# Optimization experiments

Measured on AMD Instinct MI355X. Metric: run time of the kernel, lower is better.

## Reference

```python
import jax, jax.numpy as jnp
import numpy as np

B, S, D, H = 2, 2048, 1024, 16
DEPTH = D // H
NEG = -1.0e9


def setup_inputs() -> dict:
    key = jax.random.key(0)
    ks = jax.random.split(key, 12)
    s = 1.0 / np.sqrt(D)
    return {
        "q": jax.random.normal(ks[0], (B, S, D), jnp.float32),
        "k": jax.random.normal(ks[1], (B, S, D), jnp.float32),
        "v": jax.random.normal(ks[2], (B, S, D), jnp.float32),
        "mask": jax.random.randint(ks[3], (B, 1, 1, S), 0, 2).astype(jnp.float32),
        "wq": jax.random.normal(ks[4], (D, D), jnp.float32) * s,
        "bq": jnp.zeros((D,), jnp.float32),
        "wk": jax.random.normal(ks[5], (D, D), jnp.float32) * s,
        "bk": jnp.zeros((D,), jnp.float32),
        "wv": jax.random.normal(ks[6], (D, D), jnp.float32) * s,
        "bv": jnp.zeros((D,), jnp.float32),
        "wo": jax.random.normal(ks[7], (D, D), jnp.float32) * s,
        "bo": jnp.zeros((D,), jnp.float32),
    }


def _split_heads(x):
    # [B, S, D] -> [B, H, S, depth]
    b, s, _ = x.shape
    return x.reshape(b, s, H, DEPTH).transpose(0, 2, 1, 3)


def reference(q, k, v, mask, wq, bq, wk, bk, wv, bv, wo, bo):
    qh = _split_heads(q @ wq + bq)
    kh = _split_heads(k @ wk + bk)
    vh = _split_heads(v @ wv + bv)
    scale = 1.0 / jnp.sqrt(jnp.asarray(DEPTH, jnp.float32))
    logits = jnp.einsum("bhqd,bhkd->bhqk", qh, kh) * scale
    logits = logits + mask * NEG
    attn = jax.nn.softmax(logits, axis=-1)  # [B, H, Sq, Skv]
    out = jnp.einsum("bhqk,bhkd->bhqd", attn, vh)
    out = out.transpose(0, 2, 1, 3).reshape(q.shape[0], -1, D)
    out = out @ wo + bo
    return out, attn
```

## Files before the change

### kernel.cpp

```cpp
#include <hip/hip_runtime.h>

typedef unsigned short u16;
typedef unsigned int   u32;
typedef __bf16 bf16x8 __attribute__((ext_vector_type(8)));
typedef float  f32x4  __attribute__((ext_vector_type(4)));
typedef u16    u16x8  __attribute__((ext_vector_type(8)));

#define S_   2048
#define D_   1024
#define H_   16
#define M_   4096

#define SCALE2 0.18033688011112042f
#define MASKC  (-1.4426950408889634e9f)
#define SHIFT2 11.541560327111707f

__device__ __forceinline__ u16 f2b(float f){
  union { float f; u32 i; } x; x.f = f;
  u32 u = x.i;
  u32 r = (u + 0x7fffu + ((u >> 16) & 1u)) >> 16;
  return (u16)r;
}
__device__ __forceinline__ void async16(u16* lds, const u16* g){
  __builtin_amdgcn_global_load_lds((const __attribute__((address_space(1))) void*)g,
                                   (__attribute__((address_space(3))) void*)lds, 16, 0, 0);
}
__device__ __forceinline__ f32x4 mma16(bf16x8 a, bf16x8 b, f32x4 c){
  return __builtin_amdgcn_mfma_f32_16x16x32_bf16(a, b, c, 0, 0, 0);
}
__device__ __forceinline__ bf16x8 ld_frag_u16(const u16* p){
  u16x8 v = *(const u16x8*)p;
  return __builtin_bit_cast(bf16x8, v);
}

__global__ __launch_bounds__(256) void prep(
    const float* __restrict__ q, const float* __restrict__ k, const float* __restrict__ v,
    u16* __restrict__ qb, u16* __restrict__ kb, u16* __restrict__ vb,
    const float* __restrict__ w0, const float* __restrict__ w1,
    const float* __restrict__ w2, const float* __restrict__ w3,
    u16* __restrict__ t0, u16* __restrict__ t1,
    u16* __restrict__ t2, u16* __restrict__ t3)
{
  const int bid = blockIdx.x;
  if (bid < 6144){
    const int which = bid >> 11;
    const int bx = bid & 2047;
    const float* x = (which == 0) ? q : (which == 1) ? k : v;
    u16* y = (which == 0) ? qb : (which == 1) ? kb : vb;
    size_t i = (size_t)bx * 256 + threadIdx.x;
    const f32x4* p = (const f32x4*)(x + i * 8);
    f32x4 a = p[0], b = p[1];
    u16x8 o;
    o[0] = f2b(a[0]); o[1] = f2b(a[1]); o[2] = f2b(a[2]); o[3] = f2b(a[3]);
    o[4] = f2b(b[0]); o[5] = f2b(b[1]); o[6] = f2b(b[2]); o[7] = f2b(b[3]);
    *(u16x8*)(y + i * 8) = o;
  } else {
    const int b = bid - 6144;
    const int z = b >> 8, rem = b & 255, by = rem >> 4, bx = rem & 15;
    const float* W; u16* T;
    switch (z){
      case 0: W = w0; T = t0; break;
      case 1: W = w1; T = t1; break;
      case 2: W = w2; T = t2; break;
      default: W = w3; T = t3; break;
    }
    __shared__ u16 tile[64][65];
    const int t = threadIdx.x;
    const int r0 = by * 64, c0 = bx * 64;
    const int row = t >> 2, cg = t & 3;
    const float* src = W + (size_t)(r0 + row) * D_ + c0 + cg * 16;
    f32x4 a0 = *(const f32x4*)(src + 0);
    f32x4 a1 = *(const f32x4*)(src + 4);
    f32x4 a2 = *(const f32x4*)(src + 8);
    f32x4 a3 = *(const f32x4*)(src + 12);
    #pragma unroll
    for (int e = 0; e < 4; ++e){
      tile[row][cg*16 +      e] = f2b(a0[e]);
      tile[row][cg*16 +  4 + e] = f2b(a1[e]);
      tile[row][cg*16 +  8 + e] = f2b(a2[e]);
      tile[row][cg*16 + 12 + e] = f2b(a3[e]);
    }
    __syncthreads();
    u16* dst = T + (size_t)(c0 + row) * D_ + r0 + cg * 16;
    u16x8 oa, ob;
    #pragma unroll
    for (int e = 0; e < 8; ++e){ oa[e] = tile[cg*16 + e][row]; ob[e] = tile[cg*16 + 8 + e][row]; }
    *(u16x8*)dst = oa;
    *(u16x8*)(dst + 8) = ob;
  }
}

__global__ __launch_bounds__(256) void gemm_qkv(
    const u16* __restrict__ qb, const u16* __restrict__ kb, const u16* __restrict__ vb,
    const u16* __restrict__ wqT, const u16* __restrict__ wkT, const u16* __restrict__ wvT,
    const float* __restrict__ bq, const float* __restrict__ bk, const float* __restrict__ bv,
    u16* __restrict__ Qh, u16* __restrict__ Kh, u16* __restrict__ Vt)
{
  __shared__ __attribute__((aligned(16))) u16 As[128 * 64];
  __shared__ __attribute__((aligned(16))) u16 Bs[128 * 64];
  const u16 *A, *Bt; const float* bias; u16* Cb;
  switch (blockIdx.z){
    case 0: A = qb; Bt = wqT; bias = bq; Cb = Qh; break;
    case 1: A = kb; Bt = wkT; bias = bk; Cb = Kh; break;
    default: A = vb; Bt = wvT; bias = bv; Cb = Vt; break;
  }
  const bool vtr = (blockIdx.z == 2);
  const int tid = threadIdx.x;
  const int wave = tid >> 6, lane = tid & 63, ln = lane & 15, quad = lane >> 4;
  const int wm = wave >> 1, wn = wave & 1;
  const int m0 = blockIdx.x * 128, n0 = blockIdx.y * 128;

  f32x4 acc[4][4];
  #pragma unroll
  for (int i = 0; i < 4; ++i)
    #pragma unroll
    for (int j = 0; j < 4; ++j) acc[i][j] = (f32x4){0.f, 0.f, 0.f, 0.f};

  for (int kt = 0; kt < D_; kt += 64){
    #pragma unroll
    for (int it = 0; it < 4; ++it){
      int i = it * 256 + tid;
      int r = i >> 3, c = i & 7, cs = c ^ (r & 7);
      async16(&As[i * 8], &A [(size_t)(m0 + r) * D_ + kt + cs * 8]);
      async16(&Bs[i * 8], &Bt[(size_t)(n0 + r) * D_ + kt + cs * 8]);
    }
    __syncthreads();
    #pragma unroll
    for (int kk = 0; kk < 2; ++kk){
      bf16x8 af[4], bfr[4];
      #pragma unroll
      for (int i4 = 0; i4 < 4; ++i4){
        int row = wm * 64 + i4 * 16 + ln;
        af[i4] = ld_frag_u16(&As[row * 64 + ((kk * 4 + quad) ^ (row & 7)) * 8]);
      }
      #pragma unroll
      for (int j4 = 0; j4 < 4; ++j4){
        int row = wn * 64 + j4 * 16 + ln;
        bfr[j4] = ld_frag_u16(&Bs[row * 64 + ((kk * 4 + quad) ^ (row & 7)) * 8]);
      }
      #pragma unroll
      for (int i4 = 0; i4 < 4; ++i4)
        #pragma unroll
        for (int j4 = 0; j4 < 4; ++j4)
          acc[i4][j4] = mma16(af[i4], bfr[j4], acc[i4][j4]);
    }
    __syncthreads();
  }

  #pragma unroll
  for (int j4 = 0; j4 < 4; ++j4){
    int nidx = n0 + wn * 64 + j4 * 16 + ln;
    float biasv = bias[nidx];
    #pragma unroll
    for (int i4 = 0; i4 < 4; ++i4){
      #pragma unroll
      for (int rg = 0; rg < 4; ++rg){
        int r = m0 + wm * 64 + i4 * 16 + quad * 4 + rg;
        float val = acc[i4][j4][rg] + biasv;
        int bb = r >> 11, s = r & 2047, hh = nidx >> 6, dc = nidx & 63;
        size_t idx = vtr ? (((size_t)(bb * H_ + hh) * 64 + dc) * S_ + s)
                         : (((size_t)(bb * H_ + hh) * S_ + s) * 64 + dc);
        Cb[idx] = f2b(val);
      }
    }
  }
}

__global__ __launch_bounds__(256) void gemm_o(
    const u16* __restrict__ A, const u16* __restrict__ Bt,
    const float* __restrict__ bias, float* __restrict__ Cf)
{
  __shared__ __attribute__((aligned(16))) u16 As[2][128 * 64];
  __shared__ __attribute__((aligned(16))) u16 Bs[2][128 * 64];
  const int tid = threadIdx.x;
  const int wave = tid >> 6, lane = tid & 63, ln = lane & 15, quad = lane >> 4;
  const int wm = wave >> 1, wn = wave & 1;
  const int m0 = blockIdx.x * 128, n0 = blockIdx.y * 128;

  f32x4 acc[4][4];
  #pragma unroll
  for (int i = 0; i < 4; ++i)
    #pragma unroll
    for (int j = 0; j < 4; ++j) acc[i][j] = (f32x4){0.f, 0.f, 0.f, 0.f};

  #pragma unroll
  for (int it = 0; it < 4; ++it){
    int i = it * 256 + tid;
    int r = i >> 3, c = i & 7, cs = c ^ (r & 7);
    async16(&As[0][i * 8], &A [(size_t)(m0 + r) * D_ + cs * 8]);
    async16(&Bs[0][i * 8], &Bt[(size_t)(n0 + r) * D_ + cs * 8]);
  }
  __syncthreads();

  int cur = 0;
  for (int kt = 0; kt < D_; kt += 64){
    if (kt + 64 < D_){
      int nb = cur ^ 1;
      #pragma unroll
      for (int it = 0; it < 4; ++it){
        int i = it * 256 + tid;
        int r = i >> 3, c = i & 7, cs = c ^ (r & 7);
        async16(&As[nb][i * 8], &A [(size_t)(m0 + r) * D_ + kt + 64 + cs * 8]);
        async16(&Bs[nb][i * 8], &Bt[(size_t)(n0 + r) * D_ + kt + 64 + cs * 8]);
      }
    }
    #pragma unroll
    for (int kk = 0; kk < 2; ++kk){
      bf16x8 af[4], bfr[4];
      #pragma unroll
      for (int i4 = 0; i4 < 4; ++i4){
        int row = wm * 64 + i4 * 16 + ln;
        af[i4] = ld_frag_u16(&As[cur][row * 64 + ((kk * 4 + quad) ^ (row & 7)) * 8]);
      }
      #pragma unroll
      for (int j4 = 0; j4 < 4; ++j4){
        int row = wn * 64 + j4 * 16 + ln;
        bfr[j4] = ld_frag_u16(&Bs[cur][row * 64 + ((kk * 4 + quad) ^ (row & 7)) * 8]);
      }
      #pragma unroll
      for (int i4 = 0; i4 < 4; ++i4)
        #pragma unroll
        for (int j4 = 0; j4 < 4; ++j4)
          acc[i4][j4] = mma16(af[i4], bfr[j4], acc[i4][j4]);
    }
    __syncthreads();
    cur ^= 1;
  }

  #pragma unroll
  for (int j4 = 0; j4 < 4; ++j4){
    int nidx = n0 + wn * 64 + j4 * 16 + ln;
    float biasv = bias[nidx];
    #pragma unroll
    for (int i4 = 0; i4 < 4; ++i4){
      #pragma unroll
      for (int rg = 0; rg < 4; ++rg){
        int r = m0 + wm * 64 + i4 * 16 + quad * 4 + rg;
        Cf[(size_t)r * D_ + nidx] = acc[i4][j4][rg] + biasv;
      }
    }
  }
}

__global__ __launch_bounds__(256) void attn_stats(
    const u16* __restrict__ Qh, const u16* __restrict__ Kh,
    const float* __restrict__ maskp, float* __restrict__ lrow)
{
  __shared__ __attribute__((aligned(16))) u16 Qs[64 * 64];
  __shared__ __attribute__((aligned(16))) u16 Ks[2][64 * 64];
  const int tid = threadIdx.x;
  const int wave = tid >> 6, lane = tid & 63, ln = lane & 15, quad = lane >> 4;
  const int q0 = blockIdx.x * 64;
  const int bh = blockIdx.y;
  const int bsel = bh >> 4;

  #pragma unroll
  for (int it = 0; it < 2; ++it){
    int i = it * 256 + tid;
    int r = i >> 3, c = i & 7, cs = c ^ (r & 7);
    async16(&Qs[i * 8],    &Qh[((size_t)bh * S_ + q0 + r) * 64 + cs * 8]);
    async16(&Ks[0][i * 8], &Kh[((size_t)bh * S_ + r) * 64 + cs * 8]);
  }
  __syncthreads();
  bf16x8 aq0, aq1;
  {
    int row = wave * 16 + ln;
    aq0 = ld_frag_u16(&Qs[row * 64 + ((0 + quad) ^ (row & 7)) * 8]);
    aq1 = ld_frag_u16(&Qs[row * 64 + ((4 + quad) ^ (row & 7)) * 8]);
  }

  float lsum[4] = {0.f, 0.f, 0.f, 0.f};
  int cur = 0;
  for (int n0 = 0; n0 < S_; n0 += 64){
    if (n0 + 64 < S_){
      int nb = cur ^ 1;
      #pragma unroll
      for (int it = 0; it < 2; ++it){
        int i = it * 256 + tid;
        int r = i >> 3, c = i & 7, cs = c ^ (r & 7);
        async16(&Ks[nb][i * 8], &Kh[((size_t)bh * S_ + n0 + 64 + r) * 64 + cs * 8]);
      }
    }
    float mv[4];
    #pragma unroll
    for (int j = 0; j < 4; ++j)
      mv[j] = maskp[bsel * S_ + n0 + j * 16 + ln] * MASKC - SHIFT2;
    #pragma unroll
    for (int j = 0; j < 4; ++j){
      int row = j * 16 + ln;
      bf16x8 b0 = ld_frag_u16(&Ks[cur][row * 64 + ((0 + quad) ^ (row & 7)) * 8]);
      bf16x8 b1 = ld_frag_u16(&Ks[cur][row * 64 + ((4 + quad) ^ (row & 7)) * 8]);
      f32x4 a = {0.f, 0.f, 0.f, 0.f};
      a = mma16(aq0, b0, a);
      a = mma16(aq1, b1, a);
      #pragma unroll
      for (int rg = 0; rg < 4; ++rg)
        lsum[rg] += exp2f(a[rg] * SCALE2 + mv[j]);
    }
    __syncthreads();
    cur ^= 1;
  }
  #pragma unroll
  for (int rg = 0; rg < 4; ++rg){
    float s = lsum[rg];
    s += __shfl_xor(s, 1);
    s += __shfl_xor(s, 2);
    s += __shfl_xor(s, 4);
    s += __shfl_xor(s, 8);
    if (ln == 0)
      lrow[bh * S_ + q0 + wave * 16 + quad * 4 + rg] = s;
  }
}

__global__ __launch_bounds__(256) void attn_pv(
    const u16* __restrict__ Qh, const u16* __restrict__ Kh, const u16* __restrict__ Vt,
    const float* __restrict__ maskp, const float* __restrict__ lrow,
    float* __restrict__ attn, u16* __restrict__ OH)
{
  __shared__ __attribute__((aligned(16))) u16 Qs[64 * 64];
  __shared__ __attribute__((aligned(16))) u16 Ks[2][64 * 64];
  __shared__ __attribute__((aligned(16))) u16 Vs[2][64 * 64];
  __shared__ __attribute__((aligned(16))) u16 Ps[4][16 * 72];
  const int tid = threadIdx.x;
  const int wave = tid >> 6, lane = tid & 63, ln = lane & 15, quad = lane >> 4;
  const int q0 = blockIdx.x * 64;
  const int bh = blockIdx.y;
  const int bsel = bh >> 4;

  #pragma unroll
  for (int it = 0; it < 2; ++it){
    int i = it * 256 + tid;
    int r = i >> 3, c = i & 7, cs = c ^ (r & 7);
    async16(&Qs[i * 8],    &Qh[((size_t)bh * S_ + q0 + r) * 64 + cs * 8]);
    async16(&Ks[0][i * 8], &Kh[((size_t)bh * S_ + r) * 64 + cs * 8]);
    async16(&Vs[0][i * 8], &Vt[((size_t)bh * 64 + r) * S_ + cs * 8]);
  }
  __syncthreads();
  bf16x8 aq0, aq1;
  {
    int row = wave * 16 + ln;
    aq0 = ld_frag_u16(&Qs[row * 64 + ((0 + quad) ^ (row & 7)) * 8]);
    aq1 = ld_frag_u16(&Qs[row * 64 + ((4 + quad) ^ (row & 7)) * 8]);
  }
  float il4[4];
  #pragma unroll
  for (int rg = 0; rg < 4; ++rg){
    int row = q0 + wave * 16 + quad * 4 + rg;
    il4[rg] = 1.0f / lrow[bh * S_ + row];
  }
  f32x4 oacc[4];
  #pragma unroll
  for (int jd = 0; jd < 4; ++jd) oacc[jd] = (f32x4){0.f, 0.f, 0.f, 0.f};

  int cur = 0;
  for (int n0 = 0; n0 < S_; n0 += 64){
    if (n0 + 64 < S_){
      int nb = cur ^ 1;
      #pragma unroll
      for (int it = 0; it < 2; ++it){
        int i = it * 256 + tid;
        int r = i >> 3, c = i & 7, cs = c ^ (r & 7);
        async16(&Ks[nb][i * 8], &Kh[((size_t)bh * S_ + n0 + 64 + r) * 64 + cs * 8]);
        async16(&Vs[nb][i * 8], &Vt[((size_t)bh * 64 + r) * S_ + n0 + 64 + cs * 8]);
      }
    }
    float mv[4];
    #pragma unroll
    for (int j = 0; j < 4; ++j)
      mv[j] = maskp[bsel * S_ + n0 + j * 16 + ln] * MASKC - SHIFT2;
    #pragma unroll
    for (int j = 0; j < 4; ++j){
      int row = j * 16 + ln;
      bf16x8 b0 = ld_frag_u16(&Ks[cur][row * 64 + ((0 + quad) ^ (row & 7)) * 8]);
      bf16x8 b1 = ld_frag_u16(&Ks[cur][row * 64 + ((4 + quad) ^ (row & 7)) * 8]);
      f32x4 a = {0.f, 0.f, 0.f, 0.f};
      a = mma16(aq0, b0, a);
      a = mma16(aq1, b1, a);
      #pragma unroll
      for (int rg = 0; rg < 4; ++rg){
        float p = exp2f(a[rg] * SCALE2 + mv[j]) * il4[rg];
        attn[((size_t)bh * S_ + q0 + wave * 16 + quad * 4 + rg) * S_ + n0 + j * 16 + ln] = p;
        Ps[wave][(quad * 4 + rg) * 72 + j * 16 + ln] = f2b(p);
      }
    }
    #pragma unroll
    for (int kk = 0; kk < 2; ++kk){
      bf16x8 pa = ld_frag_u16(&Ps[wave][ln * 72 + kk * 32 + quad * 8]);
      #pragma unroll
      for (int jd = 0; jd < 4; ++jd){
        int row = jd * 16 + ln;
        bf16x8 vb = ld_frag_u16(&Vs[cur][row * 64 + ((kk * 4 + quad) ^ (row & 7)) * 8]);
        oacc[jd] = mma16(pa, vb, oacc[jd]);
      }
    }
    __syncthreads();
    cur ^= 1;
  }
  const int b = bh >> 4, h = bh & 15;
  #pragma unroll
  for (int jd = 0; jd < 4; ++jd){
    #pragma unroll
    for (int rg = 0; rg < 4; ++rg){
      int row = q0 + wave * 16 + quad * 4 + rg;
      OH[((size_t)b * S_ + row) * D_ + h * 64 + jd * 16 + ln] = f2b(oacc[jd][rg]);
    }
  }
}

extern "C" void kernel_launch(void* const* d_in, const int* in_sizes, int n_in,
                              void* d_out, int out_size, void* d_ws, size_t ws_size,
                              hipStream_t stream)
{
  const float* q    = (const float*)d_in[0];
  const float* k    = (const float*)d_in[1];
  const float* v    = (const float*)d_in[2];
  const float* mask = (const float*)d_in[3];
  const float* wq   = (const float*)d_in[4];
  const float* bq   = (const float*)d_in[5];
  const float* wk   = (const float*)d_in[6];
  const float* bk   = (const float*)d_in[7];
  const float* wv   = (const float*)d_in[8];
  const float* bv   = (const float*)d_in[9];
  const float* wo   = (const float*)d_in[10];
  const float* bo   = (const float*)d_in[11];

  char* ws = (char*)d_ws;
  u16* wqT = (u16*)(ws + 0ull);
  u16* wkT = (u16*)(ws + 2097152ull);
  u16* wvT = (u16*)(ws + 4194304ull);
  u16* woT = (u16*)(ws + 6291456ull);
  u16* qb  = (u16*)(ws + 8388608ull);
  u16* kb  = (u16*)(ws + 16777216ull);
  u16* vb  = (u16*)(ws + 25165824ull);
  u16* Qh  = (u16*)(ws + 33554432ull);
  u16* Kh  = (u16*)(ws + 41943040ull);
  u16* Vt  = (u16*)(ws + 50331648ull);
  u16* OH  = (u16*)(ws + 58720256ull);
  float* lrow = (float*)(ws + 67108864ull);

  float* out  = (float*)d_out;
  float* attn = out + 4194304ull;

  prep<<<dim3(7168), 256, 0, stream>>>(q, k, v, qb, kb, vb,
                                       wq, wk, wv, wo, wqT, wkT, wvT, woT);
  gemm_qkv<<<dim3(32, 8, 3), 256, 0, stream>>>(qb, kb, vb, wqT, wkT, wvT,
                                               bq, bk, bv, Qh, Kh, Vt);
  attn_stats<<<dim3(32, 32), 256, 0, stream>>>(Qh, Kh, mask, lrow);
  attn_pv<<<dim3(32, 32), 256, 0, stream>>>(Qh, Kh, Vt, mask, lrow, attn, OH);
  gemm_o<<<dim3(32, 8), 256, 0, stream>>>(OH, woT, bo, out);
}
```

Before: 846.3 us.

## Load attention fragments directly from global memory and add separate V transpose kernel

Measured after the change: 990.1 us. 17.0% more time.

```diff
diff --git a/kernel.cpp b/kernel.cpp
--- a/kernel.cpp
+++ b/kernel.cpp
@@ -94,7 +94,7 @@
     const u16* __restrict__ qb, const u16* __restrict__ kb, const u16* __restrict__ vb,
     const u16* __restrict__ wqT, const u16* __restrict__ wkT, const u16* __restrict__ wvT,
     const float* __restrict__ bq, const float* __restrict__ bk, const float* __restrict__ bv,
-    u16* __restrict__ Qh, u16* __restrict__ Kh, u16* __restrict__ Vt)
+    u16* __restrict__ Qh, u16* __restrict__ Kh, u16* __restrict__ Vh)
 {
   __shared__ __attribute__((aligned(16))) u16 As[128 * 64];
   __shared__ __attribute__((aligned(16))) u16 Bs[128 * 64];
@@ -102,9 +102,8 @@
   switch (blockIdx.z){
     case 0: A = qb; Bt = wqT; bias = bq; Cb = Qh; break;
     case 1: A = kb; Bt = wkT; bias = bk; Cb = Kh; break;
-    default: A = vb; Bt = wvT; bias = bv; Cb = Vt; break;
-  }
-  const bool vtr = (blockIdx.z == 2);
+    default: A = vb; Bt = wvT; bias = bv; Cb = Vh; break;
+  }
   const int tid = threadIdx.x;
   const int wave = tid >> 6, lane = tid & 63, ln = lane & 15, quad = lane >> 4;
   const int wm = wave >> 1, wn = wave & 1;
@@ -158,12 +157,31 @@
         int r = m0 + wm * 64 + i4 * 16 + quad * 4 + rg;
         float val = acc[i4][j4][rg] + biasv;
         int bb = r >> 11, s = r & 2047, hh = nidx >> 6, dc = nidx & 63;
-        size_t idx = vtr ? (((size_t)(bb * H_ + hh) * 64 + dc) * S_ + s)
-                         : (((size_t)(bb * H_ + hh) * S_ + s) * 64 + dc);
-        Cb[idx] = f2b(val);
-      }
-    }
-  }
+        Cb[((size_t)(bb * H_ + hh) * S_ + s) * 64 + dc] = f2b(val);
+      }
+    }
+  }
+}
+
+__global__ __launch_bounds__(256) void vtrans(
+    const u16* __restrict__ Vh, u16* __restrict__ Vt)
+{
+  __shared__ u16 tile[64][72];
+  const int bh = blockIdx.y, s0 = blockIdx.x * 64;
+  const int t = threadIdx.x;
+  const int row = t >> 2, cg = t & 3;
+  const u16* src = Vh + ((size_t)bh * S_ + s0 + row) * 64 + cg * 16;
+  u16x8 a0 = *(const u16x8*)src;
+  u16x8 a1 = *(const u16x8*)(src + 8);
+  #pragma unroll
+  for (int e = 0; e < 8; ++e){ tile[row][cg*16 + e] = a0[e]; tile[row][cg*16 + 8 + e] = a1[e]; }
+  __syncthreads();
+  u16* dst = Vt + ((size_t)bh * 64 + row) * S_ + s0 + cg * 16;
+  u16x8 oa, ob;
+  #pragma unroll
+  for (int e = 0; e < 8; ++e){ oa[e] = tile[cg*16 + e][row]; ob[e] = tile[cg*16 + 8 + e][row]; }
+  *(u16x8*)dst = oa;
+  *(u16x8*)(dst + 8) = ob;
 }
 
 __global__ __launch_bounds__(256) void gemm_o(
@@ -246,59 +264,44 @@
     const u16* __restrict__ Qh, const u16* __restrict__ Kh,
     const float* __restrict__ maskp, float* __restrict__ lrow)
 {
-  __shared__ __attribute__((aligned(16))) u16 Qs[64 * 64];
-  __shared__ __attribute__((aligned(16))) u16 Ks[2][64 * 64];
   const int tid = threadIdx.x;
   const int wave = tid >> 6, lane = tid & 63, ln = lane & 15, quad = lane >> 4;
   const int q0 = blockIdx.x * 64;
   const int bh = blockIdx.y;
   const int bsel = bh >> 4;
 
-  #pragma unroll
-  for (int it = 0; it < 2; ++it){
-    int i = it * 256 + tid;
-    int r = i >> 3, c = i & 7, cs = c ^ (r & 7);
-    async16(&Qs[i * 8],    &Qh[((size_t)bh * S_ + q0 + r) * 64 + cs * 8]);
-    async16(&Ks[0][i * 8], &Kh[((size_t)bh * S_ + r) * 64 + cs * 8]);
-  }
-  __syncthreads();
-  bf16x8 aq0, aq1;
-  {
-    int row = wave * 16 + ln;
-    aq0 = ld_frag_u16(&Qs[row * 64 + ((0 + quad) ^ (row & 7)) * 8]);
-    aq1 = ld_frag_u16(&Qs[row * 64 + ((4 + quad) ^ (row & 7)) * 8]);
-  }
+  const u16* qp = &Qh[((size_t)bh * S_ + q0 + wave * 16 + ln) * 64 + quad * 8];
+  bf16x8 aq0 = ld_frag_u16(qp);
+  bf16x8 aq1 = ld_frag_u16(qp + 32);
+
+  const u16* kp0 = &Kh[((size_t)bh * S_ + ln) * 64 + quad * 8];
+  const u16* kp1 = kp0 + 16 * 64;
+  const u16* kp2 = kp0 + 32 * 64;
+  const u16* kp3 = kp0 + 48 * 64;
+  const float* mp = &maskp[bsel * S_ + ln];
 
   float lsum[4] = {0.f, 0.f, 0.f, 0.f};
-  int cur = 0;
   for (int n0 = 0; n0 < S_; n0 += 64){
-    if (n0 + 64 < S_){
-      int nb = cur ^ 1;
-      #pragma unroll
-      for (int it = 0; it < 2; ++it){
-        int i = it * 256 + tid;
-        int r = i >> 3, c = i & 7, cs = c ^ (r & 7);
-        async16(&Ks[nb][i * 8], &Kh[((size_t)bh * S_ + n0 + 64 + r) * 64 + cs * 8]);
-      }
-    }
-    float mv[4];
-    #pragma unroll
-    for (int j = 0; j < 4; ++j)
-      mv[j] = maskp[bsel * S_ + n0 + j * 16 + ln] * MASKC - SHIFT2;
-    #pragma unroll
-    for (int j = 0; j < 4; ++j){
-      int row = j * 16 + ln;
-      bf16x8 b0 = ld_frag_u16(&Ks[cur][row * 64 + ((0 + quad) ^ (row & 7)) * 8]);
-      bf16x8 b1 = ld_frag_u16(&Ks[cur][row * 64 + ((4 + quad) ^ (row & 7)) * 8]);
-      f32x4 a = {0.f, 0.f, 0.f, 0.f};
-      a = mma16(aq0, b0, a);
-      a = mma16(aq1, b1, a);
-      #pragma unroll
-      for (int rg = 0; rg < 4; ++rg)
-        lsum[rg] += exp2f(a[rg] * SCALE2 + mv[j]);
-    }
-    __syncthreads();
-    cur ^= 1;
+    float mv0 = mp[ 0] * MASKC - SHIFT2;
+    float mv1 = mp[16] * MASKC - SHIFT2;
+    float mv2 = mp[32] * MASKC - SHIFT2;
+    float mv3 = mp[48] * MASKC - SHIFT2;
+    bf16x8 b00 = ld_frag_u16(kp0), b01 = ld_frag_u16(kp0 + 32);
+    bf16x8 b10 = ld_frag_u16(kp1), b11 = ld_frag_u16(kp1 + 32);
+    bf16x8 b20 = ld_frag_u16(kp2), b21 = ld_frag_u16(kp2 + 32);
+    bf16x8 b30 = ld_frag_u16(kp3), b31 = ld_frag_u16(kp3 + 32);
+    f32x4 a0 = {0.f,0.f,0.f,0.f}, a1 = a0, a2 = a0, a3 = a0;
+    a0 = mma16(aq0, b00, a0); a0 = mma16(aq1, b01, a0);
+    a1 = mma16(aq0, b10, a1); a1 = mma16(aq1, b11, a1);
+    a2 = mma16(aq0, b20, a2); a2 = mma16(aq1, b21, a2);
+    a3 = mma16(aq0, b30, a3); a3 = mma16(aq1, b31, a3);
+    #pragma unroll
+    for (int rg = 0; rg < 4; ++rg){
+      lsum[rg] += exp2f(a0[rg] * SCALE2 + mv0) + exp2f(a1[rg] * SCALE2 + mv1)
+                + exp2f(a2[rg] * SCALE2 + mv2) + exp2f(a3[rg] * SCALE2 + mv3);
+    }
+    kp0 += 64 * 64; kp1 += 64 * 64; kp2 += 64 * 64; kp3 += 64 * 64;
+    mp += 64;
   }
   #pragma unroll
   for (int rg = 0; rg < 4; ++rg){
@@ -317,9 +320,6 @@
     const float* __restrict__ maskp, const float* __restrict__ lrow,
     float* __restrict__ attn, u16* __restrict__ OH)
 {
-  __shared__ __attribute__((aligned(16))) u16 Qs[64 * 64];
-  __shared__ __attribute__((aligned(16))) u16 Ks[2][64 * 64];
-  __shared__ __attribute__((aligned(16))) u16 Vs[2][64 * 64];
   __shared__ __attribute__((aligned(16))) u16 Ps[4][16 * 72];
   const int tid = threadIdx.x;
   const int wave = tid >> 6, lane = tid & 63, ln = lane & 15, quad = lane >> 4;
@@ -327,21 +327,10 @@
   const int bh = blockIdx.y;
   const int bsel = bh >> 4;
 
-  #pragma unroll
-  for (int it = 0; it < 2; ++it){
-    int i = it * 256 + tid;
-    int r = i >> 3, c = i & 7, cs = c ^ (r & 7);
-    async16(&Qs[i * 8],    &Qh[((size_t)bh * S_ + q0 + r) * 64 + cs * 8]);
-    async16(&Ks[0][i * 8], &Kh[((size_t)bh * S_ + r) * 64 + cs * 8]);
-    async16(&Vs[0][i * 8], &Vt[((size_t)bh * 64 + r) * S_ + cs * 8]);
-  }
-  __syncthreads();
-  bf16x8 aq0, aq1;
-  {
-    int row = wave * 16 + ln;
-    aq0 = ld_frag_u16(&Qs[row * 64 + ((0 + quad) ^ (row & 7)) * 8]);
-    aq1 = ld_frag_u16(&Qs[row * 64 + ((4 + quad) ^ (row & 7)) * 8]);
-  }
+  const u16* qp = &Qh[((size_t)bh * S_ + q0 + wave * 16 + ln) * 64 + quad * 8];
+  bf16x8 aq0 = ld_frag_u16(qp);
+  bf16x8 aq1 = ld_frag_u16(qp + 32);
+
   float il4[4];
   #pragma unroll
   for (int rg = 0; rg < 4; ++rg){
@@ -352,49 +341,58 @@
   #pragma unroll
   for (int jd = 0; jd < 4; ++jd) oacc[jd] = (f32x4){0.f, 0.f, 0.f, 0.f};
 
-  int cur = 0;
+  const u16* kp0 = &Kh[((size_t)bh * S_ + ln) * 64 + quad * 8];
+  const u16* kp1 = kp0 + 16 * 64;
+  const u16* kp2 = kp0 + 32 * 64;
+  const u16* kp3 = kp0 + 48 * 64;
+  const u16* vp0 = &Vt[((size_t)bh * 64 + ln) * S_ + quad * 8];
+  const u16* vp1 = vp0 + (size_t)16 * S_;
+  const u16* vp2 = vp0 + (size_t)32 * S_;
+  const u16* vp3 = vp0 + (size_t)48 * S_;
+  const float* mp = &maskp[bsel * S_ + ln];
+  float* ap = &attn[((size_t)bh * S_ + q0 + wave * 16 + quad * 4) * S_ + ln];
+  u16* psw = &Ps[wave][(quad * 4) * 72 + ln];
+  const u16* psr = &Ps[wave][ln * 72 + quad * 8];
+
   for (int n0 = 0; n0 < S_; n0 += 64){
-    if (n0 + 64 < S_){
-      int nb = cur ^ 1;
-      #pragma unroll
-      for (int it = 0; it < 2; ++it){
-        int i = it * 256 + tid;
-        int r = i >> 3, c = i & 7, cs = c ^ (r & 7);
-        async16(&Ks[nb][i * 8], &Kh[((size_t)bh * S_ + n0 + 64 + r) * 64 + cs * 8]);
-        async16(&Vs[nb][i * 8], &Vt[((size_t)bh * 64 + r) * S_ + n0 + 64 + cs * 8]);
-      }
-    }
-    float mv[4];
-    #pragma unroll
-    for (int j = 0; j < 4; ++j)
-      mv[j] = maskp[bsel * S_ + n0 + j * 16 + ln] * MASKC - SHIFT2;
-    #pragma unroll
-    for (int j = 0; j < 4; ++j){
-      int row = j * 16 + ln;
-      bf16x8 b0 = ld_frag_u16(&Ks[cur][row * 64 + ((0 + quad) ^ (row & 7)) * 8]);
-      bf16x8 b1 = ld_frag_u16(&Ks[cur][row * 64 + ((4 + quad) ^ (row & 7)) * 8]);
-      f32x4 a = {0.f, 0.f, 0.f, 0.f};
-      a = mma16(aq0, b0, a);
-      a = mma16(aq1, b1, a);
-      #pragma unroll
-      for (int rg = 0; rg < 4; ++rg){
-        float p = exp2f(a[rg] * SCALE2 + mv[j]) * il4[rg];
-        attn[((size_t)bh * S_ + q0 + wave * 16 + quad * 4 + rg) * S_ + n0 + j * 16 + ln] = p;
-        Ps[wave][(quad * 4 + rg) * 72 + j * 16 + ln] = f2b(p);
-      }
+    float mv0 = mp[ 0] * MASKC - SHIFT2;
+    float mv1 = mp[16] * MASKC - SHIFT2;
+    float mv2 = mp[32] * MASKC - SHIFT2;
+    float mv3 = mp[48] * MASKC - SHIFT2;
+    bf16x8 b00 = ld_frag_u16(kp0), b01 = ld_frag_u16(kp0 + 32);
+    bf16x8 b10 = ld_frag_u16(kp1), b11 = ld_frag_u16(kp1 + 32);
+    bf16x8 b20 = ld_frag_u16(kp2), b21 = ld_frag_u16(kp2 + 32);
+    bf16x8 b30 = ld_frag_u16(kp3), b31 = ld_frag_u16(kp3 + 32);
+    f32x4 a0 = {0.f,0.f,0.f,0.f}, a1 = a0, a2 = a0, a3 = a0;
+    a0 = mma16(aq0, b00, a0); a0 = mma16(aq1, b01, a0);
+    a1 = mma16(aq0, b10, a1); a1 = mma16(aq1, b11, a1);
+    a2 = mma16(aq0, b20, a2); a2 = mma16(aq1, b21, a2);
+    a3 = mma16(aq0, b30, a3); a3 = mma16(aq1, b31, a3);
+    #pragma unroll
+    for (int rg = 0; rg < 4; ++rg){
+      float p0 = exp2f(a0[rg] * SCALE2 + mv0) * il4[rg];
+      float p1 = exp2f(a1[rg] * SCALE2 + mv1) * il4[rg];
+      float p2 = exp2f(a2[rg] * SCALE2 + mv2) * il4[rg];
+      float p3 = exp2f(a3[rg] * SCALE2 + mv3) * il4[rg];
+      float* arow = ap + (size_t)rg * S_ + n0;
+      arow[ 0] = p0; arow[16] = p1; arow[32] = p2; arow[48] = p3;
+      u16* pr = psw + rg * 72;
+      pr[ 0] = f2b(p0); pr[16] = f2b(p1); pr[32] = f2b(p2); pr[48] = f2b(p3);
     }
     #pragma unroll
     for (int kk = 0; kk < 2; ++kk){
-      bf16x8 pa = ld_frag_u16(&Ps[wave][ln * 72 + kk * 32 + quad * 8]);
-      #pragma unroll
-      for (int jd = 0; jd < 4; ++jd){
-        int row = jd * 16 + ln;
-        bf16x8 vb = ld_frag_u16(&Vs[cur][row * 64 + ((kk * 4 + quad) ^ (row & 7)) * 8]);
-        oacc[jd] = mma16(pa, vb, oacc[jd]);
-      }
-    }
-    __syncthreads();
-    cur ^= 1;
+      bf16x8 pa = ld_frag_u16(psr + kk * 32);
+      bf16x8 v0 = ld_frag_u16(vp0 + n0 + kk * 32);
+      bf16x8 v1 = ld_frag_u16(vp1 + n0 + kk * 32);
+      bf16x8 v2 = ld_frag_u16(vp2 + n0 + kk * 32);
+      bf16x8 v3 = ld_frag_u16(vp3 + n0 + kk * 32);
+      oacc[0] = mma16(pa, v0, oacc[0]);
+      oacc[1] = mma16(pa, v1, oacc[1]);
+      oacc[2] = mma16(pa, v2, oacc[2]);
+      oacc[3] = mma16(pa, v3, oacc[3]);
+    }
+    kp0 += 64 * 64; kp1 += 64 * 64; kp2 += 64 * 64; kp3 += 64 * 64;
+    mp += 64;
   }
   const int b = bh >> 4, h = bh & 15;
   #pragma unroll
@@ -434,9 +432,10 @@
   u16* vb  = (u16*)(ws + 25165824ull);
   u16* Qh  = (u16*)(ws + 33554432ull);
   u16* Kh  = (u16*)(ws + 41943040ull);
-  u16* Vt  = (u16*)(ws + 50331648ull);
+  u16* Vh  = (u16*)(ws + 50331648ull);
   u16* OH  = (u16*)(ws + 58720256ull);
   float* lrow = (float*)(ws + 67108864ull);
+  u16* Vt  = vb;
 
   float* out  = (float*)d_out;
   float* attn = out + 4194304ull;
@@ -444,7 +443,8 @@
   prep<<<dim3(7168), 256, 0, stream>>>(q, k, v, qb, kb, vb,
                                        wq, wk, wv, wo, wqT, wkT, wvT, woT);
   gemm_qkv<<<dim3(32, 8, 3), 256, 0, stream>>>(qb, kb, vb, wqT, wkT, wvT,
-                                               bq, bk, bv, Qh, Kh, Vt);
+                                               bq, bk, bv, Qh, Kh, Vh);
+  vtrans<<<dim3(32, 32), 256, 0, stream>>>(Vh, Vt);
   attn_stats<<<dim3(32, 32), 256, 0, stream>>>(Qh, Kh, mask, lrow);
   attn_pv<<<dim3(32, 32), 256, 0, stream>>>(Qh, Kh, Vt, mask, lrow, attn, OH);
   gemm_o<<<dim3(32, 8), 256, 0, stream>>>(OH, woT, bo, out);
```

## Double attention query tile, remap blocks per XCD, and stage QKV epilogue via LDS

Applied to the files above, without the earlier changes.

After: 810.5 us. 1.04x faster.

```diff
diff --git a/kernel.cpp b/kernel.cpp
--- a/kernel.cpp
+++ b/kernel.cpp
@@ -96,8 +96,9 @@
     const float* __restrict__ bq, const float* __restrict__ bk, const float* __restrict__ bv,
     u16* __restrict__ Qh, u16* __restrict__ Kh, u16* __restrict__ Vt)
 {
-  __shared__ __attribute__((aligned(16))) u16 As[128 * 64];
-  __shared__ __attribute__((aligned(16))) u16 Bs[128 * 64];
+  __shared__ __attribute__((aligned(16))) u16 smem[128 * 132];
+  u16* As = smem;
+  u16* Bs = smem + 128 * 64;
   const u16 *A, *Bt; const float* bias; u16* Cb;
   switch (blockIdx.z){
     case 0: A = qb; Bt = wqT; bias = bq; Cb = Qh; break;
@@ -149,19 +150,32 @@
 
   #pragma unroll
   for (int j4 = 0; j4 < 4; ++j4){
-    int nidx = n0 + wn * 64 + j4 * 16 + ln;
-    float biasv = bias[nidx];
+    int nl = wn * 64 + j4 * 16 + ln;
+    float biasv = bias[n0 + nl];
     #pragma unroll
     for (int i4 = 0; i4 < 4; ++i4){
       #pragma unroll
       for (int rg = 0; rg < 4; ++rg){
-        int r = m0 + wm * 64 + i4 * 16 + quad * 4 + rg;
-        float val = acc[i4][j4][rg] + biasv;
-        int bb = r >> 11, s = r & 2047, hh = nidx >> 6, dc = nidx & 63;
-        size_t idx = vtr ? (((size_t)(bb * H_ + hh) * 64 + dc) * S_ + s)
-                         : (((size_t)(bb * H_ + hh) * S_ + s) * 64 + dc);
-        Cb[idx] = f2b(val);
-      }
+        int ml = wm * 64 + i4 * 16 + quad * 4 + rg;
+        u16 hv = f2b(acc[i4][j4][rg] + biasv);
+        smem[vtr ? (nl * 132 + ml) : (ml * 132 + nl)] = hv;
+      }
+    }
+  }
+  __syncthreads();
+  const int bb = m0 >> 11, sbase = m0 & 2047;
+  #pragma unroll
+  for (int c = 0; c < 8; ++c){
+    int task = c * 256 + tid;
+    int rr = task >> 4, ch = task & 15;
+    u16x8 val = *(const u16x8*)&smem[rr * 132 + ch * 8];
+    if (vtr){
+      int hh = (n0 + rr) >> 6, dc = (n0 + rr) & 63;
+      *(u16x8*)&Cb[((size_t)(bb * H_ + hh) * 64 + dc) * S_ + sbase + ch * 8] = val;
+    } else {
+      int s = sbase + rr;
+      int nn = n0 + ch * 8, hh = nn >> 6, dc = nn & 63;
+      *(u16x8*)&Cb[((size_t)(bb * H_ + hh) * S_ + s) * 64 + dc] = val;
     }
   }
 }
@@ -246,30 +260,38 @@
     const u16* __restrict__ Qh, const u16* __restrict__ Kh,
     const float* __restrict__ maskp, float* __restrict__ lrow)
 {
-  __shared__ __attribute__((aligned(16))) u16 Qs[64 * 64];
+  __shared__ __attribute__((aligned(16))) u16 Qs[128 * 64];
   __shared__ __attribute__((aligned(16))) u16 Ks[2][64 * 64];
   const int tid = threadIdx.x;
   const int wave = tid >> 6, lane = tid & 63, ln = lane & 15, quad = lane >> 4;
-  const int q0 = blockIdx.x * 64;
-  const int bh = blockIdx.y;
+  const int orig = blockIdx.x;
+  const int xcd = orig & 7, slot = orig >> 3;
+  const int bh = xcd * 4 + (slot >> 4);
+  const int q0 = (slot & 15) * 128;
   const int bsel = bh >> 4;
 
+  #pragma unroll
+  for (int it = 0; it < 4; ++it){
+    int i = it * 256 + tid;
+    int r = i >> 3, c = i & 7, cs = c ^ (r & 7);
+    async16(&Qs[i * 8], &Qh[((size_t)bh * S_ + q0 + r) * 64 + cs * 8]);
+  }
   #pragma unroll
   for (int it = 0; it < 2; ++it){
     int i = it * 256 + tid;
     int r = i >> 3, c = i & 7, cs = c ^ (r & 7);
-    async16(&Qs[i * 8],    &Qh[((size_t)bh * S_ + q0 + r) * 64 + cs * 8]);
     async16(&Ks[0][i * 8], &Kh[((size_t)bh * S_ + r) * 64 + cs * 8]);
   }
   __syncthreads();
-  bf16x8 aq0, aq1;
-  {
-    int row = wave * 16 + ln;
-    aq0 = ld_frag_u16(&Qs[row * 64 + ((0 + quad) ^ (row & 7)) * 8]);
-    aq1 = ld_frag_u16(&Qs[row * 64 + ((4 + quad) ^ (row & 7)) * 8]);
-  }
-
-  float lsum[4] = {0.f, 0.f, 0.f, 0.f};
+  bf16x8 aq[2][2];
+  #pragma unroll
+  for (int f = 0; f < 2; ++f){
+    int row = wave * 32 + f * 16 + ln;
+    aq[f][0] = ld_frag_u16(&Qs[row * 64 + ((0 + quad) ^ (row & 7)) * 8]);
+    aq[f][1] = ld_frag_u16(&Qs[row * 64 + ((4 + quad) ^ (row & 7)) * 8]);
+  }
+
+  float lsum[2][4] = {{0.f,0.f,0.f,0.f},{0.f,0.f,0.f,0.f}};
   int cur = 0;
   for (int n0 = 0; n0 < S_; n0 += 64){
     if (n0 + 64 < S_){
@@ -290,26 +312,31 @@
       int row = j * 16 + ln;
       bf16x8 b0 = ld_frag_u16(&Ks[cur][row * 64 + ((0 + quad) ^ (row & 7)) * 8]);
       bf16x8 b1 = ld_frag_u16(&Ks[cur][row * 64 + ((4 + quad) ^ (row & 7)) * 8]);
-      f32x4 a = {0.f, 0.f, 0.f, 0.f};
-      a = mma16(aq0, b0, a);
-      a = mma16(aq1, b1, a);
-      #pragma unroll
-      for (int rg = 0; rg < 4; ++rg)
-        lsum[rg] += exp2f(a[rg] * SCALE2 + mv[j]);
+      #pragma unroll
+      for (int f = 0; f < 2; ++f){
+        f32x4 a = {0.f, 0.f, 0.f, 0.f};
+        a = mma16(aq[f][0], b0, a);
+        a = mma16(aq[f][1], b1, a);
+        #pragma unroll
+        for (int rg = 0; rg < 4; ++rg)
+          lsum[f][rg] += exp2f(a[rg] * SCALE2 + mv[j]);
+      }
     }
     __syncthreads();
     cur ^= 1;
   }
   #pragma unroll
-  for (int rg = 0; rg < 4; ++rg){
-    float s = lsum[rg];
-    s += __shfl_xor(s, 1);
-    s += __shfl_xor(s, 2);
-    s += __shfl_xor(s, 4);
-    s += __shfl_xor(s, 8);
-    if (ln == 0)
-      lrow[bh * S_ + q0 + wave * 16 + quad * 4 + rg] = s;
-  }
+  for (int f = 0; f < 2; ++f)
+    #pragma unroll
+    for (int rg = 0; rg < 4; ++rg){
+      float s = lsum[f][rg];
+      s += __shfl_xor(s, 1);
+      s += __shfl_xor(s, 2);
+      s += __shfl_xor(s, 4);
+      s += __shfl_xor(s, 8);
+      if (ln == 0)
+        lrow[bh * S_ + q0 + wave * 32 + f * 16 + quad * 4 + rg] = s;
+    }
 }
 
 __global__ __launch_bounds__(256) void attn_pv(
@@ -317,40 +344,46 @@
     const float* __restrict__ maskp, const float* __restrict__ lrow,
     float* __restrict__ attn, u16* __restrict__ OH)
 {
-  __shared__ __attribute__((aligned(16))) u16 Qs[64 * 64];
   __shared__ __attribute__((aligned(16))) u16 Ks[2][64 * 64];
   __shared__ __attribute__((aligned(16))) u16 Vs[2][64 * 64];
-  __shared__ __attribute__((aligned(16))) u16 Ps[4][16 * 72];
+  __shared__ __attribute__((aligned(16))) u16 Ps[4][32 * 72];
   const int tid = threadIdx.x;
   const int wave = tid >> 6, lane = tid & 63, ln = lane & 15, quad = lane >> 4;
-  const int q0 = blockIdx.x * 64;
-  const int bh = blockIdx.y;
+  const int orig = blockIdx.x;
+  const int xcd = orig & 7, slot = orig >> 3;
+  const int bh = xcd * 4 + (slot >> 4);
+  const int q0 = (slot & 15) * 128;
   const int bsel = bh >> 4;
+
+  bf16x8 aq[2][2];
+  #pragma unroll
+  for (int f = 0; f < 2; ++f){
+    const u16* qp = &Qh[((size_t)bh * S_ + q0 + wave * 32 + f * 16 + ln) * 64 + quad * 8];
+    aq[f][0] = ld_frag_u16(qp);
+    aq[f][1] = ld_frag_u16(qp + 32);
+  }
+  float il[2][4];
+  #pragma unroll
+  for (int f = 0; f < 2; ++f)
+    #pragma unroll
+    for (int rg = 0; rg < 4; ++rg){
+      int row = q0 + wave * 32 + f * 16 + quad * 4 + rg;
+      il[f][rg] = 1.0f / lrow[bh * S_ + row];
+    }
+  f32x4 oacc[2][4];
+  #pragma unroll
+  for (int f = 0; f < 2; ++f)
+    #pragma unroll
+    for (int jd = 0; jd < 4; ++jd) oacc[f][jd] = (f32x4){0.f, 0.f, 0.f, 0.f};
 
   #pragma unroll
   for (int it = 0; it < 2; ++it){
     int i = it * 256 + tid;
     int r = i >> 3, c = i & 7, cs = c ^ (r & 7);
-    async16(&Qs[i * 8],    &Qh[((size_t)bh * S_ + q0 + r) * 64 + cs * 8]);
     async16(&Ks[0][i * 8], &Kh[((size_t)bh * S_ + r) * 64 + cs * 8]);
     async16(&Vs[0][i * 8], &Vt[((size_t)bh * 64 + r) * S_ + cs * 8]);
   }
   __syncthreads();
-  bf16x8 aq0, aq1;
-  {
-    int row = wave * 16 + ln;
-    aq0 = ld_frag_u16(&Qs[row * 64 + ((0 + quad) ^ (row & 7)) * 8]);
-    aq1 = ld_frag_u16(&Qs[row * 64 + ((4 + quad) ^ (row & 7)) * 8]);
-  }
-  float il4[4];
-  #pragma unroll
-  for (int rg = 0; rg < 4; ++rg){
-    int row = q0 + wave * 16 + quad * 4 + rg;
-    il4[rg] = 1.0f / lrow[bh * S_ + row];
-  }
-  f32x4 oacc[4];
-  #pragma unroll
-  for (int jd = 0; jd < 4; ++jd) oacc[jd] = (f32x4){0.f, 0.f, 0.f, 0.f};
 
   int cur = 0;
   for (int n0 = 0; n0 < S_; n0 += 64){
@@ -373,38 +406,45 @@
       int row = j * 16 + ln;
       bf16x8 b0 = ld_frag_u16(&Ks[cur][row * 64 + ((0 + quad) ^ (row & 7)) * 8]);
       bf16x8 b1 = ld_frag_u16(&Ks[cur][row * 64 + ((4 + quad) ^ (row & 7)) * 8]);
-      f32x4 a = {0.f, 0.f, 0.f, 0.f};
-      a = mma16(aq0, b0, a);
-      a = mma16(aq1, b1, a);
+      #pragma unroll
+      for (int f = 0; f < 2; ++f){
+        f32x4 a = {0.f, 0.f, 0.f, 0.f};
+        a = mma16(aq[f][0], b0, a);
+        a = mma16(aq[f][1], b1, a);
+        #pragma unroll
+        for (int rg = 0; rg < 4; ++rg){
+          float p = exp2f(a[rg] * SCALE2 + mv[j]) * il[f][rg];
+          attn[((size_t)bh * S_ + q0 + wave * 32 + f * 16 + quad * 4 + rg) * S_ + n0 + j * 16 + ln] = p;
+          Ps[wave][(f * 16 + quad * 4 + rg) * 72 + j * 16 + ln] = f2b(p);
+        }
+      }
+    }
+    #pragma unroll
+    for (int f = 0; f < 2; ++f){
+      #pragma unroll
+      for (int kk = 0; kk < 2; ++kk){
+        bf16x8 pa = ld_frag_u16(&Ps[wave][(f * 16 + ln) * 72 + kk * 32 + quad * 8]);
+        #pragma unroll
+        for (int jd = 0; jd < 4; ++jd){
+          int row = jd * 16 + ln;
+          bf16x8 vb = ld_frag_u16(&Vs[cur][row * 64 + ((kk * 4 + quad) ^ (row & 7)) * 8]);
+          oacc[f][jd] = mma16(pa, vb, oacc[f][jd]);
+        }
+      }
+    }
+    __syncthreads();
+    cur ^= 1;
+  }
+  const int b = bh >> 4, h = bh & 15;
+  #pragma unroll
+  for (int f = 0; f < 2; ++f)
+    #pragma unroll
+    for (int jd = 0; jd < 4; ++jd)
       #pragma unroll
       for (int rg = 0; rg < 4; ++rg){
-        float p = exp2f(a[rg] * SCALE2 + mv[j]) * il4[rg];
-        attn[((size_t)bh * S_ + q0 + wave * 16 + quad * 4 + rg) * S_ + n0 + j * 16 + ln] = p;
-        Ps[wave][(quad * 4 + rg) * 72 + j * 16 + ln] = f2b(p);
-      }
-    }
-    #pragma unroll
-    for (int kk = 0; kk < 2; ++kk){
-      bf16x8 pa = ld_frag_u16(&Ps[wave][ln * 72 + kk * 32 + quad * 8]);
-      #pragma unroll
-      for (int jd = 0; jd < 4; ++jd){
-        int row = jd * 16 + ln;
-        bf16x8 vb = ld_frag_u16(&Vs[cur][row * 64 + ((kk * 4 + quad) ^ (row & 7)) * 8]);
-        oacc[jd] = mma16(pa, vb, oacc[jd]);
-      }
-    }
-    __syncthreads();
-    cur ^= 1;
-  }
-  const int b = bh >> 4, h = bh & 15;
-  #pragma unroll
-  for (int jd = 0; jd < 4; ++jd){
-    #pragma unroll
-    for (int rg = 0; rg < 4; ++rg){
-      int row = q0 + wave * 16 + quad * 4 + rg;
-      OH[((size_t)b * S_ + row) * D_ + h * 64 + jd * 16 + ln] = f2b(oacc[jd][rg]);
-    }
-  }
+        int row = q0 + wave * 32 + f * 16 + quad * 4 + rg;
+        OH[((size_t)b * S_ + row) * D_ + h * 64 + jd * 16 + ln] = f2b(oacc[f][jd][rg]);
+      }
 }
 
 extern "C" void kernel_launch(void* const* d_in, const int* in_sizes, int n_in,
@@ -445,7 +485,7 @@
                                        wq, wk, wv, wo, wqT, wkT, wvT, woT);
   gemm_qkv<<<dim3(32, 8, 3), 256, 0, stream>>>(qb, kb, vb, wqT, wkT, wvT,
                                                bq, bk, bv, Qh, Kh, Vt);
-  attn_stats<<<dim3(32, 32), 256, 0, stream>>>(Qh, Kh, mask, lrow);
-  attn_pv<<<dim3(32, 32), 256, 0, stream>>>(Qh, Kh, Vt, mask, lrow, attn, OH);
+  attn_stats<<<dim3(512), 256, 0, stream>>>(Qh, Kh, mask, lrow);
+  attn_pv<<<dim3(512), 256, 0, stream>>>(Qh, Kh, Vt, mask, lrow, attn, OH);
   gemm_o<<<dim3(32, 8), 256, 0, stream>>>(OH, woT, bo, out);
 }
```
